# Optimization experiments

Measured on AMD Instinct MI355X. Metric: run time of the kernel, lower is better.

Reference implementation:

```python
import jax, jax.numpy as jnp
import numpy as np

HIDDEN = 2048
HEADS = 16
HEAD_DIM = HIDDEN // HEADS


def setup_inputs() -> dict:
    key = jax.random.key(0)
    kx, kq, kk, kv, ko = jax.random.split(key, 5)
    s = 1.0 / np.sqrt(HIDDEN)
    return {
        "x": jax.random.normal(kx, (2, 2048, HIDDEN), dtype=jnp.float32),
        "Wq": jax.random.normal(kq, (HIDDEN, HIDDEN), dtype=jnp.float32) * s,
        "Wk": jax.random.normal(kk, (HIDDEN, HIDDEN), dtype=jnp.float32) * s,
        "Wv": jax.random.normal(kv, (HIDDEN, HIDDEN), dtype=jnp.float32) * s,
        "Wo": jax.random.normal(ko, (HIDDEN, HIDDEN), dtype=jnp.float32) * s,
    }


def reference(x, Wq, Wk, Wv, Wo):
    B, S, H = x.shape
    nh, hd = HEADS, HEAD_DIM
    # projections (nn.Linear: y = x @ W.T; here W stored as [in, out] so x @ W)
    q = (x @ Wq).reshape(B, S, nh, hd).transpose(0, 2, 1, 3)  # [B,nh,S,hd]
    k = (x @ Wk).reshape(B, S, nh, hd).transpose(0, 2, 1, 3)
    v = (x @ Wv).reshape(B, S, nh, hd).transpose(0, 2, 1, 3)
    scores = jnp.einsum("bhqd,bhkd->bhqk", q, k) / jnp.sqrt(jnp.float32(hd))
    causal = jnp.tril(jnp.ones((S, S), dtype=bool))  # keep lower triangle
    scores = jnp.where(causal, scores, jnp.finfo(scores.dtype).min)
    attn = jax.nn.softmax(scores, axis=-1)
    out = jnp.einsum("bhqk,bhkd->bhqd", attn, v)
    out = out.transpose(0, 2, 1, 3).reshape(B, S, H)
    return out @ Wo
```

## Files before the change

### kernel.cpp

```cpp
#include <hip/hip_runtime.h>
#include <stdint.h>

typedef unsigned short u16;
typedef __bf16 bf16x8 __attribute__((ext_vector_type(8)));
typedef short s4 __attribute__((ext_vector_type(4)));
typedef float f32x4 __attribute__((ext_vector_type(4)));

#define B_ 2
#define S_ 2048
#define H_ 2048
#define NH_ 16
#define HD_ 128

#define SL2f (0.08838834764831845f * 1.4426950408889634f)

__device__ __forceinline__ u16 f2bf(float f) {
    uint32_t u = __float_as_uint(f);
    u += 0x7fff + ((u >> 16) & 1);
    return (u16)(u >> 16);
}

__device__ __forceinline__ uint32_t pk_bf16(float lo, float hi) {
    return __builtin_amdgcn_perm(__float_as_uint(hi), __float_as_uint(lo), 0x07060302u);
}

__device__ __forceinline__ void gl_lds16(const u16* g, u16* l) {
    __builtin_amdgcn_global_load_lds(
        (const __attribute__((address_space(1))) void*)g,
        (__attribute__((address_space(3))) void*)l, 16, 0, 0);
}

union U2S4 { uint2 u; s4 s; };

__global__ __launch_bounds__(256) void cast_x_kernel(const float* __restrict__ x, u16* __restrict__ xb) {
    int i = (blockIdx.x * 256 + threadIdx.x) * 4;
    float4 v = *(const float4*)&x[i];
    ushort4 o;
    o.x = f2bf(v.x); o.y = f2bf(v.y); o.z = f2bf(v.z); o.w = f2bf(v.w);
    *(ushort4*)&xb[i] = o;
}

__global__ __launch_bounds__(256) void transpose_cast_kernel(
        const float* __restrict__ w0, const float* __restrict__ w1,
        const float* __restrict__ w2, const float* __restrict__ w3,
        u16* __restrict__ dqkv, u16* __restrict__ dwo) {
    int z = blockIdx.z;
    const float* src = (z == 0) ? w0 : (z == 1) ? w1 : (z == 2) ? w2 : w3;
    u16* dst = (z < 3) ? (dqkv + (size_t)z * H_ * H_) : dwo;
    __shared__ float tile[32][33];
    int n0 = blockIdx.x * 32, k0 = blockIdx.y * 32;
    int tx = threadIdx.x, ty = threadIdx.y;
#pragma unroll
    for (int i = 0; i < 4; i++)
        tile[ty + i * 8][tx] = src[(size_t)(k0 + ty + i * 8) * H_ + n0 + tx];
    __syncthreads();
#pragma unroll
    for (int i = 0; i < 4; i++)
        dst[(size_t)(n0 + ty + i * 8) * H_ + k0 + tx] = f2bf(tile[tx][ty + i * 8]);
}

template <int MODE>
__global__ __launch_bounds__(256, 2) void gemm_bt(
        const u16* __restrict__ A, const u16* __restrict__ Bt, float* __restrict__ Cout,
        u16* __restrict__ q, u16* __restrict__ k, u16* __restrict__ v,
        int M, int N, int K) {
    __shared__ u16 sm[2 * 128 * 64];
    u16* As = sm;
    u16* Bs = sm + 128 * 64;
    int tid = threadIdx.x;
    int w = tid >> 6, lane = tid & 63, quad = lane >> 4, l16 = lane & 15;
    int wm = w >> 1, wn = w & 1;
    int m0 = blockIdx.y * 128, n0 = blockIdx.x * 128;

    f32x4 acc[4][4];
#pragma unroll
    for (int mi = 0; mi < 4; mi++)
#pragma unroll
        for (int ni = 0; ni < 4; ni++)
            acc[mi][ni] = (f32x4){0.f, 0.f, 0.f, 0.f};

    for (int k0 = 0; k0 < K; k0 += 64) {
        const u16* ga = A + (size_t)m0 * K + k0;
        const u16* gb = Bt + (size_t)n0 * K + k0;
#pragma unroll
        for (int j = 0; j < 4; j++) {
            int base = (j * 4 + w) * 64;
            int p = base + lane;
            int row = p >> 3;
            int c = (p & 7) ^ (row & 7);
            gl_lds16(&ga[(size_t)row * K + c * 8], &As[base * 8]);
            gl_lds16(&gb[(size_t)row * K + c * 8], &Bs[base * 8]);
        }
        __syncthreads();
#pragma unroll
        for (int ks = 0; ks < 2; ks++) {
            bf16x8 af[4], bf[4];
#pragma unroll
            for (int mi = 0; mi < 4; mi++) {
                int row = wm * 64 + mi * 16 + l16;
                af[mi] = *(const bf16x8*)&As[row * 64 + (((ks * 4 + quad) ^ (row & 7)) * 8)];
            }
#pragma unroll
            for (int ni = 0; ni < 4; ni++) {
                int row = wn * 64 + ni * 16 + l16;
                bf[ni] = *(const bf16x8*)&Bs[row * 64 + (((ks * 4 + quad) ^ (row & 7)) * 8)];
            }
#pragma unroll
            for (int mi = 0; mi < 4; mi++)
#pragma unroll
                for (int ni = 0; ni < 4; ni++)
                    acc[mi][ni] = __builtin_amdgcn_mfma_f32_16x16x32_bf16(af[mi], bf[ni], acc[mi][ni], 0, 0, 0);
        }
        __syncthreads();
    }

    if (MODE == 0 && n0 >= 4096) {
#pragma unroll
        for (int mi = 0; mi < 4; mi++) {
#pragma unroll
            for (int ni = 0; ni < 4; ni++) {
                int nl = wn * 64 + ni * 16 + l16;
#pragma unroll
                for (int r = 0; r < 4; r++) {
                    int ml = wm * 64 + mi * 16 + quad * 4 + r;
                    sm[nl * 128 + (((ml >> 3) ^ (nl & 15)) * 8) + (ml & 7)] = f2bf(acc[mi][ni][r]);
                }
            }
        }
        __syncthreads();
        int b = m0 >> 11, s0 = m0 & 2047;
#pragma unroll
        for (int i = 0; i < 8; i++) {
            int cu = tid + i * 256;
            int nl = cu >> 4, mc = cu & 15;
            int4 val = *(const int4*)&sm[nl * 128 + ((mc ^ (nl & 15)) * 8)];
            int ngl = (n0 - 4096) + nl;
            int h = ngl >> 7, d = ngl & 127;
            *(int4*)&v[((size_t)((b * NH_ + h) * HD_ + d)) * S_ + s0 + mc * 8] = val;
        }
    } else {
#pragma unroll
        for (int mi = 0; mi < 4; mi++) {
#pragma unroll
            for (int ni = 0; ni < 4; ni++) {
                int ng = n0 + wn * 64 + ni * 16 + l16;
#pragma unroll
                for (int r = 0; r < 4; r++) {
                    int mg = m0 + wm * 64 + mi * 16 + quad * 4 + r;
                    float val = acc[mi][ni][r];
                    if (MODE == 0) {
                        int which = ng >> 11;
                        int rem = ng & 2047;
                        int h = rem >> 7, d = rem & 127;
                        int b = mg >> 11, s = mg & 2047;
                        if (which == 0)
                            q[((size_t)((b * NH_ + h) * S_ + s)) * HD_ + d] = f2bf(val * SL2f);
                        else
                            k[((size_t)((b * NH_ + h) * S_ + s)) * HD_ + d] = f2bf(val);
                    } else {
                        Cout[(size_t)mg * N + ng] = val;
                    }
                }
            }
        }
    }
}

__global__ __launch_bounds__(256, 3) void flash_kernel(
        const u16* __restrict__ Q, const u16* __restrict__ Kb,
        const u16* __restrict__ VT, u16* __restrict__ Ctx) {
    __shared__ u16 Ks[2][64 * 128];
    __shared__ u16 Vs[128 * 64];
    int tid = threadIdx.x;
    int w = tid >> 6, lane = tid & 63, quad = lane >> 4, l16 = lane & 15;

    int id = blockIdx.x;
    int bh = id & 31;
    int b = bh >> 4, h = bh & 15;
    int qt = 31 - (id >> 5);
    int q0 = qt * 64;

    size_t bhoff = ((size_t)b * NH_ + h) * S_ * HD_;
    const u16* Qp = Q + bhoff;
    const u16* Kp = Kb + bhoff;
    const u16* Vp = VT + bhoff;

    auto stageK = [&](int t, int buf) {
        int kv0 = t * 64;
#pragma unroll
        for (int j = 0; j < 4; j++) {
            int base = (j * 4 + w) * 64;
            int p = base + lane;
            int row = p >> 4;
            int c = (p & 15) ^ (row & 15);
            gl_lds16(&Kp[(size_t)(kv0 + row) * HD_ + c * 8], &Ks[buf][base * 8]);
        }
    };
    auto stageV = [&](int t) {
        int kv0 = t * 64;
#pragma unroll
        for (int j = 0; j < 4; j++) {
            int base = (j * 4 + w) * 64;
            int p = base + lane;
            int row = p >> 3;
            int c = (p & 7) ^ (row & 7);
            gl_lds16(&Vp[(size_t)row * S_ + kv0 + c * 8], &Vs[base * 8]);
        }
    };

    int qw = q0 + w * 16;
    int qg = qw + l16;
    bf16x8 qf[4];
#pragma unroll
    for (int ks = 0; ks < 4; ks++)
        qf[ks] = *(const bf16x8*)&Qp[(size_t)qg * HD_ + ks * 32 + quad * 8];

    float l_part = 0.f;
    f32x4 ao[8];
#pragma unroll
    for (int dt = 0; dt < 8; dt++) ao[dt] = (f32x4){0.f, 0.f, 0.f, 0.f};

    stageK(0, 0);

    for (int t = 0; t <= qt; t++) {
        int buf = t & 1;
        __syncthreads();
        if (t < qt) stageK(t + 1, (t + 1) & 1);
        stageV(t);

        f32x4 sc[4];
#pragma unroll
        for (int nt = 0; nt < 4; nt++) {
            sc[nt] = (f32x4){0.f, 0.f, 0.f, 0.f};
            int row = nt * 16 + l16;
#pragma unroll
            for (int ks = 0; ks < 4; ks++) {
                bf16x8 kf = *(const bf16x8*)&Ks[buf][row * 128 + (((ks * 4 + quad) ^ (row & 15)) * 8)];
                sc[nt] = __builtin_amdgcn_mfma_f32_16x16x32_bf16(kf, qf[ks], sc[nt], 0, 0, 0);
            }
        }

        U2S4 pk[4];
        if (t < qt) {
#pragma unroll
            for (int nt = 0; nt < 4; nt++) {
                float p0 = exp2f(sc[nt][0]), p1 = exp2f(sc[nt][1]);
                float p2 = exp2f(sc[nt][2]), p3 = exp2f(sc[nt][3]);
                l_part += (p0 + p1) + (p2 + p3);
                pk[nt].u.x = pk_bf16(p0, p1);
                pk[nt].u.y = pk_bf16(p2, p3);
            }
        } else {
            int kvb = t * 64 + quad * 4;
#pragma unroll
            for (int nt = 0; nt < 4; nt++) {
                int kv = kvb + nt * 16;
                float p0 = (kv + 0 > qg) ? 0.f : exp2f(sc[nt][0]);
                float p1 = (kv + 1 > qg) ? 0.f : exp2f(sc[nt][1]);
                float p2 = (kv + 2 > qg) ? 0.f : exp2f(sc[nt][2]);
                float p3 = (kv + 3 > qg) ? 0.f : exp2f(sc[nt][3]);
                l_part += (p0 + p1) + (p2 + p3);
                pk[nt].u.x = pk_bf16(p0, p1);
                pk[nt].u.y = pk_bf16(p2, p3);
            }
        }

        __syncthreads();

#pragma unroll
        for (int kt = 0; kt < 4; kt++) {
#pragma unroll
            for (int dt = 0; dt < 8; dt++) {
                int d = dt * 16 + l16;
                int c = kt * 2 + (quad >> 1);
                s4 va = *(const s4*)&Vs[d * 64 + ((c ^ (d & 7)) * 8) + (quad & 1) * 4];
                ao[dt] = __builtin_amdgcn_mfma_f32_16x16x16bf16_1k(va, pk[kt].s, ao[dt], 0, 0, 0);
            }
        }
    }

    float l = l_part;
    l += __shfl_xor(l, 16);
    l += __shfl_xor(l, 32);
    float inv = 1.0f / l;
    size_t base = ((size_t)b * S_ + qg) * H_ + h * HD_;
#pragma unroll
    for (int dt = 0; dt < 8; dt++) {
        float a0 = ao[dt][0] * inv, a1 = ao[dt][1] * inv;
        float a2 = ao[dt][2] * inv, a3 = ao[dt][3] * inv;
        uint2 st;
        st.x = pk_bf16(a0, a1);
        st.y = pk_bf16(a2, a3);
        *(uint2*)&Ctx[base + dt * 16 + quad * 4] = st;
    }
}

extern "C" void kernel_launch(void* const* d_in, const int* in_sizes, int n_in,
                              void* d_out, int out_size, void* d_ws, size_t ws_size,
                              hipStream_t stream) {
    const float* x  = (const float*)d_in[0];
    const float* Wq = (const float*)d_in[1];
    const float* Wk = (const float*)d_in[2];
    const float* Wv = (const float*)d_in[3];
    const float* Wo = (const float*)d_in[4];
    float* out = (float*)d_out;

    const size_t MB = 1024 * 1024;
    char* ws = (char*)d_ws;
    u16* Xb    = (u16*)(ws);
    u16* WqkvT = (u16*)(ws + 16 * MB);
    u16* WoT   = (u16*)(ws + 40 * MB);
    u16* Qb    = (u16*)(ws + 48 * MB);
    u16* Kbuf  = (u16*)(ws + 64 * MB);
    u16* VT    = (u16*)(ws + 80 * MB);
    u16* Ctx   = (u16*)(ws + 96 * MB);

    cast_x_kernel<<<8192, 256, 0, stream>>>(x, Xb);
    transpose_cast_kernel<<<dim3(64, 64, 4), dim3(32, 8), 0, stream>>>(Wq, Wk, Wv, Wo, WqkvT, WoT);
    gemm_bt<0><<<dim3(48, 32), 256, 0, stream>>>(Xb, WqkvT, nullptr, Qb, Kbuf, VT, 4096, 6144, 2048);
    flash_kernel<<<1024, 256, 0, stream>>>(Qb, Kbuf, VT, Ctx);
    gemm_bt<1><<<dim3(16, 32), 256, 0, stream>>>(Ctx, WoT, out, nullptr, nullptr, nullptr, 4096, 2048, 2048);
}
```

Baseline: 354.2 us.

## Pair causal query tiles per flash block, double-buffer V, merge prep kernels

Each flash block now processes two query tiles (a short one and its complementary long one), so every block does exactly 33 KV iterations and causal load imbalance goes away; the grid shrinks from 1024 to 512 blocks. V is now double-buffered alongside K, and the prefetch of the next K/V tile moves after the QK MFMAs with an extra barrier. Occupancy hint drops to 2 blocks per CU because LDS use grows. The x cast and the weight transpose/cast kernels are merged into one launch to cut launch overhead.

```diff
diff --git a/kernel.cpp b/kernel.cpp
--- a/kernel.cpp
+++ b/kernel.cpp
@@ -32,24 +32,29 @@
 
 union U2S4 { uint2 u; s4 s; };
 
-__global__ __launch_bounds__(256) void cast_x_kernel(const float* __restrict__ x, u16* __restrict__ xb) {
-    int i = (blockIdx.x * 256 + threadIdx.x) * 4;
-    float4 v = *(const float4*)&x[i];
-    ushort4 o;
-    o.x = f2bf(v.x); o.y = f2bf(v.y); o.z = f2bf(v.z); o.w = f2bf(v.w);
-    *(ushort4*)&xb[i] = o;
-}
-
-__global__ __launch_bounds__(256) void transpose_cast_kernel(
+__global__ __launch_bounds__(256) void prep_kernel(
+        const float* __restrict__ x,
         const float* __restrict__ w0, const float* __restrict__ w1,
         const float* __restrict__ w2, const float* __restrict__ w3,
-        u16* __restrict__ dqkv, u16* __restrict__ dwo) {
+        u16* __restrict__ xb, u16* __restrict__ dqkv, u16* __restrict__ dwo) {
     int z = blockIdx.z;
+    int tx = threadIdx.x, ty = threadIdx.y;
+    if (z == 4) {
+        int tid = ty * 32 + tx;
+        size_t base = ((size_t)(blockIdx.y * 64 + blockIdx.x)) * 2048 + tid * 8;
+#pragma unroll
+        for (int i = 0; i < 2; i++) {
+            float4 v = *(const float4*)&x[base + i * 4];
+            ushort4 o;
+            o.x = f2bf(v.x); o.y = f2bf(v.y); o.z = f2bf(v.z); o.w = f2bf(v.w);
+            *(ushort4*)&xb[base + i * 4] = o;
+        }
+        return;
+    }
     const float* src = (z == 0) ? w0 : (z == 1) ? w1 : (z == 2) ? w2 : w3;
     u16* dst = (z < 3) ? (dqkv + (size_t)z * H_ * H_) : dwo;
     __shared__ float tile[32][33];
     int n0 = blockIdx.x * 32, k0 = blockIdx.y * 32;
-    int tx = threadIdx.x, ty = threadIdx.y;
 #pragma unroll
     for (int i = 0; i < 4; i++)
         tile[ty + i * 8][tx] = src[(size_t)(k0 + ty + i * 8) * H_ + n0 + tx];
@@ -166,19 +171,20 @@
     }
 }
 
-__global__ __launch_bounds__(256, 3) void flash_kernel(
+__global__ __launch_bounds__(256, 2) void flash_kernel(
         const u16* __restrict__ Q, const u16* __restrict__ Kb,
         const u16* __restrict__ VT, u16* __restrict__ Ctx) {
     __shared__ u16 Ks[2][64 * 128];
-    __shared__ u16 Vs[128 * 64];
+    __shared__ u16 Vs[2][128 * 64];
     int tid = threadIdx.x;
     int w = tid >> 6, lane = tid & 63, quad = lane >> 4, l16 = lane & 15;
 
     int id = blockIdx.x;
     int bh = id & 31;
     int b = bh >> 4, h = bh & 15;
-    int qt = 31 - (id >> 5);
-    int q0 = qt * 64;
+    int pair = id >> 5;
+    int qts = pair, qtl = 31 - pair;
+    int n0 = qts + 1;
 
     size_t bhoff = ((size_t)b * NH_ + h) * S_ * HD_;
     const u16* Qp = Q + bhoff;
@@ -186,7 +192,7 @@
     const u16* Vp = VT + bhoff;
 
     auto stageK = [&](int t, int buf) {
-        int kv0 = t * 64;
+        int kv0 = ((t >= n0) ? (t - n0) : t) * 64;
 #pragma unroll
         for (int j = 0; j < 4; j++) {
             int base = (j * 4 + w) * 64;
@@ -196,20 +202,20 @@
             gl_lds16(&Kp[(size_t)(kv0 + row) * HD_ + c * 8], &Ks[buf][base * 8]);
         }
     };
-    auto stageV = [&](int t) {
-        int kv0 = t * 64;
+    auto stageV = [&](int t, int buf) {
+        int kv0 = ((t >= n0) ? (t - n0) : t) * 64;
 #pragma unroll
         for (int j = 0; j < 4; j++) {
             int base = (j * 4 + w) * 64;
             int p = base + lane;
             int row = p >> 3;
             int c = (p & 7) ^ (row & 7);
-            gl_lds16(&Vp[(size_t)row * S_ + kv0 + c * 8], &Vs[base * 8]);
+            gl_lds16(&Vp[(size_t)row * S_ + kv0 + c * 8], &Vs[buf][base * 8]);
         }
     };
 
-    int qw = q0 + w * 16;
-    int qg = qw + l16;
+    int q0 = qts * 64;
+    int qg = q0 + w * 16 + l16;
     bf16x8 qf[4];
 #pragma unroll
     for (int ks = 0; ks < 4; ks++)
@@ -220,13 +226,40 @@
 #pragma unroll
     for (int dt = 0; dt < 8; dt++) ao[dt] = (f32x4){0.f, 0.f, 0.f, 0.f};
 
+    auto epilogue = [&]() {
+        float l = l_part;
+        l += __shfl_xor(l, 16);
+        l += __shfl_xor(l, 32);
+        float inv = 1.0f / l;
+        size_t base = ((size_t)b * S_ + qg) * H_ + h * HD_;
+#pragma unroll
+        for (int dt = 0; dt < 8; dt++) {
+            u16 o0 = f2bf(ao[dt][0] * inv), o1 = f2bf(ao[dt][1] * inv);
+            u16 o2 = f2bf(ao[dt][2] * inv), o3 = f2bf(ao[dt][3] * inv);
+            uint2 st;
+            st.x = (uint32_t)o0 | ((uint32_t)o1 << 16);
+            st.y = (uint32_t)o2 | ((uint32_t)o3 << 16);
+            *(uint2*)&Ctx[base + dt * 16 + quad * 4] = st;
+        }
+    };
+
     stageK(0, 0);
-
-    for (int t = 0; t <= qt; t++) {
+    stageV(0, 0);
+
+    for (int t = 0; t < 33; t++) {
+        if (t == n0) {
+            epilogue();
+            q0 = qtl * 64;
+            qg = q0 + w * 16 + l16;
+#pragma unroll
+            for (int ks = 0; ks < 4; ks++)
+                qf[ks] = *(const bf16x8*)&Qp[(size_t)qg * HD_ + ks * 32 + quad * 8];
+            l_part = 0.f;
+#pragma unroll
+            for (int dt = 0; dt < 8; dt++) ao[dt] = (f32x4){0.f, 0.f, 0.f, 0.f};
+        }
         int buf = t & 1;
         __syncthreads();
-        if (t < qt) stageK(t + 1, (t + 1) & 1);
-        stageV(t);
 
         f32x4 sc[4];
 #pragma unroll
@@ -240,8 +273,16 @@
             }
         }
 
+        __syncthreads();
+
+        if (t + 1 < 33) {
+            stageK(t + 1, buf ^ 1);
+            stageV(t + 1, buf ^ 1);
+        }
+
+        bool diag = (t == n0 - 1) || (t == 32);
         U2S4 pk[4];
-        if (t < qt) {
+        if (!diag) {
 #pragma unroll
             for (int nt = 0; nt < 4; nt++) {
                 float p0 = exp2f(sc[nt][0]), p1 = exp2f(sc[nt][1]);
@@ -251,7 +292,7 @@
                 pk[nt].u.y = pk_bf16(p2, p3);
             }
         } else {
-            int kvb = t * 64 + quad * 4;
+            int kvb = q0 + quad * 4;
 #pragma unroll
             for (int nt = 0; nt < 4; nt++) {
                 int kv = kvb + nt * 16;
@@ -265,34 +306,18 @@
             }
         }
 
-        __syncthreads();
-
 #pragma unroll
         for (int kt = 0; kt < 4; kt++) {
 #pragma unroll
             for (int dt = 0; dt < 8; dt++) {
                 int d = dt * 16 + l16;
                 int c = kt * 2 + (quad >> 1);
-                s4 va = *(const s4*)&Vs[d * 64 + ((c ^ (d & 7)) * 8) + (quad & 1) * 4];
+                s4 va = *(const s4*)&Vs[buf][d * 64 + ((c ^ (d & 7)) * 8) + (quad & 1) * 4];
                 ao[dt] = __builtin_amdgcn_mfma_f32_16x16x16bf16_1k(va, pk[kt].s, ao[dt], 0, 0, 0);
             }
         }
     }
-
-    float l = l_part;
-    l += __shfl_xor(l, 16);
-    l += __shfl_xor(l, 32);
-    float inv = 1.0f / l;
-    size_t base = ((size_t)b * S_ + qg) * H_ + h * HD_;
-#pragma unroll
-    for (int dt = 0; dt < 8; dt++) {
-        float a0 = ao[dt][0] * inv, a1 = ao[dt][1] * inv;
-        float a2 = ao[dt][2] * inv, a3 = ao[dt][3] * inv;
-        uint2 st;
-        st.x = pk_bf16(a0, a1);
-        st.y = pk_bf16(a2, a3);
-        *(uint2*)&Ctx[base + dt * 16 + quad * 4] = st;
-    }
+    epilogue();
 }
 
 extern "C" void kernel_launch(void* const* d_in, const int* in_sizes, int n_in,
@@ -315,9 +340,8 @@
     u16* VT    = (u16*)(ws + 80 * MB);
     u16* Ctx   = (u16*)(ws + 96 * MB);
 
-    cast_x_kernel<<<8192, 256, 0, stream>>>(x, Xb);
-    transpose_cast_kernel<<<dim3(64, 64, 4), dim3(32, 8), 0, stream>>>(Wq, Wk, Wv, Wo, WqkvT, WoT);
+    prep_kernel<<<dim3(64, 64, 5), dim3(32, 8), 0, stream>>>(x, Wq, Wk, Wv, Wo, Xb, WqkvT, WoT);
     gemm_bt<0><<<dim3(48, 32), 256, 0, stream>>>(Xb, WqkvT, nullptr, Qb, Kbuf, VT, 4096, 6144, 2048);
-    flash_kernel<<<1024, 256, 0, stream>>>(Qb, Kbuf, VT, Ctx);
+    flash_kernel<<<512, 256, 0, stream>>>(Qb, Kbuf, VT, Ctx);
     gemm_bt<1><<<dim3(16, 32), 256, 0, stream>>>(Ctx, WoT, out, nullptr, nullptr, nullptr, 4096, 2048, 2048);
 }
```

New measurement: 331.0 us. 1.07x faster.
